# Kernel tuning notes

Hardware: AMD Instinct MI355X
Metric: run time of the kernel (lower is better)

Reference implementation:

```python
import jax, jax.numpy as jnp
import numpy as np

U, I, R, D = 100000, 50000, 5, 64
E_UI, E_UU = 1000000, 500000


def leaky(x, s):
    return jnp.where(x > 0, x, s * x)


def edge_softmax(scores, seg, n):
    # softmax over edges grouped by destination node (DGL edge_softmax)
    m = jax.ops.segment_max(scores, seg, num_segments=n)
    e = jnp.exp(scores - m[seg])
    s = jax.ops.segment_sum(e, seg, num_segments=n)
    return e / s[seg]


def attention(src, dst, w1, b1, w2, b2, w3, b3):
    # Attention module: relu(att1(cat)) -> relu(att2) -> att3 (dropout off: eval mode)
    x = jnp.concatenate([src, dst], axis=1)
    x = jax.nn.relu(x @ w1 + b1)
    x = jax.nn.relu(x @ w2 + b2)
    return (x @ w3 + b3)[:, 0]  # [E]


def setup_inputs() -> dict:
    key = jax.random.key(0)
    ks = iter(jax.random.split(key, 64))
    def p(*shape):
        return jax.random.normal(next(ks), shape, jnp.float32) * 0.05
    inp = {
        'user_emb': p(U, D), 'item_emb': p(I, D), 'rating_emb': p(R, D),
        'gv_w1': p(2 * D, D), 'gv_b1': p(D), 'gv_w2': p(D, D), 'gv_b2': p(D),
        'attI_w1': p(2 * D, D), 'attI_b1': p(D), 'attI_w2': p(D, D), 'attI_b2': p(D), 'attI_w3': p(D, 1), 'attI_b3': p(1),
        'wI_w': p(D, D), 'wI_b': p(D),
        'attS_w1': p(2 * D, D), 'attS_b1': p(D), 'attS_w2': p(D, D), 'attS_b2': p(D), 'attS_w3': p(D, 1), 'attS_b3': p(1),
        'wS_w': p(D, D), 'wS_b': p(D),
        'W2_w': p(2 * D, D), 'W2_b': p(D),
        'gu_w1': p(2 * D, D), 'gu_b1': p(D), 'gu_w2': p(D, D), 'gu_b2': p(D),
        'attU_w1': p(2 * D, D), 'attU_b1': p(D), 'attU_w2': p(D, D), 'attU_b2': p(D), 'attU_w3': p(D, 1), 'attU_b3': p(1),
        'wU_w': p(D, D), 'wU_b': p(D),
        'user_e': jax.random.randint(next(ks), (E_UI,), 0, U, jnp.int32),
        'item_e': jax.random.randint(next(ks), (E_UI,), 0, I, jnp.int32),
        'rating_e': jax.random.randint(next(ks), (E_UI,), 0, R, jnp.int32),
        'trust_e': jax.random.randint(next(ks), (E_UU,), 0, U, jnp.int32),
        'trustee_e': jax.random.randint(next(ks), (E_UU,), 0, U, jnp.int32),
    }
    return inp


def reference(user_emb, item_emb, rating_emb,
              gv_w1, gv_b1, gv_w2, gv_b2,
              attI_w1, attI_b1, attI_w2, attI_b2, attI_w3, attI_b3,
              wI_w, wI_b,
              attS_w1, attS_b1, attS_w2, attS_b2, attS_w3, attS_b3,
              wS_w, wS_b,
              W2_w, W2_b,
              gu_w1, gu_b1, gu_w2, gu_b2,
              attU_w1, attU_b1, attU_w2, attU_b2, attU_w3, attU_b3,
              wU_w, wU_b,
              user_e, item_e, rating_e, trust_e, trustee_e):
    act = lambda x: leaky(x, 0.2)  # LeakyReLU(0.2)

    # ---- ItemAgg: item->user edges, edge softmax over destination users ----
    i_e = item_emb[item_e]                     # [E_ui, D]
    u_e = user_emb[user_e]
    r_e = rating_emb[rating_e]
    x = jnp.concatenate([i_e, r_e], axis=1)    # gv MLP: LeakyReLU(0.01) default
    x = leaky(x @ gv_w1 + gv_b1, 0.01)
    x_ia = leaky(x @ gv_w2 + gv_b2, 0.01)
    sc = attention(x_ia, u_e, attI_w1, attI_b1, attI_w2, attI_b2, attI_w3, attI_b3)
    val = edge_softmax(sc, user_e, U)
    h = jax.ops.segment_sum(x_ia * val[:, None], user_e, num_segments=U)  # [U, D]
    hI = act(h @ wI_w + wI_b)

    # ---- SocialAgg: trust->trustee edges, softmax per trustee ----
    tr_e = user_emb[trust_e]
    te_e = hI[trustee_e]
    sc = attention(tr_e, te_e, attS_w1, attS_b1, attS_w2, attS_b2, attS_w3, attS_b3)
    val = edge_softmax(sc, trustee_e, U)
    # A.T @ hI: aggregate hi[trust] into trustee nodes with edge weights
    agg = jax.ops.segment_sum(val[:, None] * hI[trust_e], trustee_e, num_segments=U)
    hS = act(agg @ wS_w + wS_b)

    h_out = act(jnp.concatenate([hI, hS], axis=1) @ W2_w + W2_b)  # [U, D]

    # ---- UserAgg: user->item edges, softmax per destination item ----
    x = jnp.concatenate([user_emb[user_e], r_e], axis=1)
    x = jax.nn.relu(x @ gu_w1 + gu_b1)
    f_jt = jax.nn.relu(x @ gu_w2 + gu_b2)
    sc = attention(f_jt, i_e, attU_w1, attU_b1, attU_w2, attU_b2, attU_w3, attU_b3)
    val = edge_softmax(sc, item_e, I)
    z = jax.ops.segment_sum(f_jt * val[:, None], item_e, num_segments=I)  # [I, D]
    z = act(z @ wU_w + wU_b)

    return (h_out, z)
```

## Files before the change

### kernel.cpp

```cpp
#include <hip/hip_runtime.h>


typedef unsigned int   u32;
typedef unsigned short u16;
typedef short bf16x8 __attribute__((ext_vector_type(8)));
typedef float f32x4  __attribute__((ext_vector_type(4)));

#define U_N   100000
#define I_N   50000
#define EUI_E 1000000
#define EUU_E 500000
#define DOUT_ROWS 300000
#define RANGE 256
#define PB    256

__device__ __forceinline__ float bflo(u32 u){ return __uint_as_float(u << 16); }
__device__ __forceinline__ float bfhi(u32 u){ return __uint_as_float(u & 0xffff0000u); }
__device__ __forceinline__ u16 f2bf(float f){
  u32 x = __float_as_uint(f);
  x += 0x7fffu + ((x >> 16) & 1u);
  return (u16)(x >> 16);
}
__device__ __forceinline__ u32 pk2(float a, float b){
  return (u32)f2bf(a) | ((u32)f2bf(b) << 16);
}
__device__ __forceinline__ float actf(float x, float s){ return fmaxf(x, x * s); }
__device__ __forceinline__ void cvt8(uint4 q, float f[8]){
  f[0]=bflo(q.x); f[1]=bfhi(q.x); f[2]=bflo(q.y); f[3]=bfhi(q.y);
  f[4]=bflo(q.z); f[5]=bfhi(q.z); f[6]=bflo(q.w); f[7]=bfhi(q.w);
}

__device__ __forceinline__ bf16x8 bfrag(const float* __restrict__ W, int kt, int nt, int l){
  int c = l & 15, g = l >> 4;
  const float* p = W + (size_t)(kt*32 + g*8) * 64 + nt*16 + c;
  bf16x8 r;
  #pragma unroll
  for (int j = 0; j < 8; ++j) r[j] = (short)f2bf(p[(size_t)j * 64]);
  return r;
}
__device__ __forceinline__ bf16x8 afrag_f32(const float* p){
  float4 a = *(const float4*)p, b = *(const float4*)(p + 4);
  bf16x8 r;
  r[0]=(short)f2bf(a.x); r[1]=(short)f2bf(a.y); r[2]=(short)f2bf(a.z); r[3]=(short)f2bf(a.w);
  r[4]=(short)f2bf(b.x); r[5]=(short)f2bf(b.y); r[6]=(short)f2bf(b.z); r[7]=(short)f2bf(b.w);
  return r;
}
__device__ __forceinline__ bf16x8 afrag_f32s(const float* p, float s){
  float4 a = *(const float4*)p, b = *(const float4*)(p + 4);
  bf16x8 r;
  r[0]=(short)f2bf(a.x*s); r[1]=(short)f2bf(a.y*s); r[2]=(short)f2bf(a.z*s); r[3]=(short)f2bf(a.w*s);
  r[4]=(short)f2bf(b.x*s); r[5]=(short)f2bf(b.y*s); r[6]=(short)f2bf(b.z*s); r[7]=(short)f2bf(b.w*s);
  return r;
}
#define LDT 68
__device__ __forceinline__ void dwrite(float* lb, const f32x4* acc, float slope, int l){
  int c = l & 15, g = l >> 4;
  #pragma unroll
  for (int nt = 0; nt < 4; ++nt){
    #pragma unroll
    for (int rg = 0; rg < 4; ++rg)
      lb[(4*g + rg)*LDT + nt*16 + c] = actf(acc[nt][rg], slope);
  }
}
__device__ __forceinline__ bf16x8 afrag_lds(const float* lb, int kt, int l){
  int r = l & 15, g = l >> 4;
  return afrag_f32(lb + r*LDT + kt*32 + g*8);
}
__device__ __forceinline__ void store_rows2(const float* lb, u16* lo, u16* hi, int ndout,
                                            int base, int nrows, int l){
  int r = l >> 2, q = l & 3;
  if (r >= nrows) return;
  int row = base + r;
  u16* out = (row < ndout) ? lo + (size_t)row * 64 : hi + (size_t)(row - ndout) * 64;
  const float* src = lb + r*LDT + q*16;
  float4 a = *(const float4*)src, b = *(const float4*)(src+4);
  float4 c = *(const float4*)(src+8), d = *(const float4*)(src+12);
  uint4 w0, w1;
  w0.x = pk2(a.x,a.y); w0.y = pk2(a.z,a.w); w0.z = pk2(b.x,b.y); w0.w = pk2(b.z,b.w);
  w1.x = pk2(c.x,c.y); w1.y = pk2(c.z,c.w); w1.z = pk2(d.x,d.y); w1.w = pk2(d.z,d.w);
  u32* dst = (u32*)(out + (size_t)q*16);
  *(uint4*)dst = w0;
  *(uint4*)(dst + 4) = w1;
}
__device__ __forceinline__ void store_rows_f32(const float* lb, float* out,
                                               int base, int nrows, int l){
  int r = l >> 2, q = l & 3;
  if (r >= nrows) return;
  const float* src = lb + r*LDT + q*16;
  float* dst = out + (size_t)(base + r)*64 + q*16;
  *(float4*)(dst)    = *(const float4*)(src);
  *(float4*)(dst+4)  = *(const float4*)(src+4);
  *(float4*)(dst+8)  = *(const float4*)(src+8);
  *(float4*)(dst+12) = *(const float4*)(src+12);
}
#define MFMA(a,b,c) __builtin_amdgcn_mfma_f32_16x16x32_bf16((a),(b),(c),0,0,0)

__global__ void __launch_bounds__(256) mfma_pair_k(
    const float* __restrict__ embA, const float* __restrict__ embR,
    const float* __restrict__ W1, const float* __restrict__ b1,
    const float* __restrict__ W2, const float* __restrict__ b2,
    float slope, int plo, int phi, u16* __restrict__ Xlo, u16* __restrict__ Xhi, int ndout)
{
  __shared__ float lbuf[4][16*LDT];
  int l   = threadIdx.x & 63;
  int wid = threadIdx.x >> 6;
  float* lb = lbuf[wid];
  int c = l & 15;
  bf16x8 w1f[4][4], w2f[2][4];
  #pragma unroll
  for (int kt = 0; kt < 4; ++kt)
    #pragma unroll
    for (int nt = 0; nt < 4; ++nt) w1f[kt][nt] = bfrag(W1, kt, nt, l);
  #pragma unroll
  for (int kt = 0; kt < 2; ++kt)
    #pragma unroll
    for (int nt = 0; nt < 4; ++nt) w2f[kt][nt] = bfrag(W2, kt, nt, l);
  float bias1[4], bias2[4];
  #pragma unroll
  for (int nt = 0; nt < 4; ++nt){ bias1[nt] = b1[nt*16 + c]; bias2[nt] = b2[nt*16 + c]; }

  int n = phi - plo;
  int ngrp = (n + 15) >> 4;
  for (int grp = blockIdx.x*4 + wid; grp < ngrp; grp += gridDim.x*4){
    int base = grp * 16;
    int p = plo + base + (l & 15);
    if (p >= phi) p = phi - 1;
    int i = p / 5, r = p - 5*i;
    const float* ra = embA + (size_t)i * 64;
    const float* rr = embR + (size_t)r * 64;
    bf16x8 a0 = afrag_f32(ra + (l>>4)*8);
    bf16x8 a1 = afrag_f32(ra + 32 + (l>>4)*8);
    bf16x8 a2 = afrag_f32(rr + (l>>4)*8);
    bf16x8 a3 = afrag_f32(rr + 32 + (l>>4)*8);
    f32x4 acc[4];
    #pragma unroll
    for (int nt = 0; nt < 4; ++nt){
      f32x4 v; v[0]=bias1[nt]; v[1]=bias1[nt]; v[2]=bias1[nt]; v[3]=bias1[nt];
      v = MFMA(a0, w1f[0][nt], v);
      v = MFMA(a1, w1f[1][nt], v);
      v = MFMA(a2, w1f[2][nt], v);
      v = MFMA(a3, w1f[3][nt], v);
      acc[nt] = v;
    }
    dwrite(lb, acc, slope, l);
    bf16x8 x0 = afrag_lds(lb, 0, l);
    bf16x8 x1 = afrag_lds(lb, 1, l);
    #pragma unroll
    for (int nt = 0; nt < 4; ++nt){
      f32x4 v; v[0]=bias2[nt]; v[1]=bias2[nt]; v[2]=bias2[nt]; v[3]=bias2[nt];
      v = MFMA(x0, w2f[0][nt], v);
      v = MFMA(x1, w2f[1][nt], v);
      acc[nt] = v;
    }
    dwrite(lb, acc, slope, l);
    int nrows = n - base; if (nrows > 16) nrows = 16;
    store_rows2(lb, Xlo, Xhi, ndout, base, nrows, l);
  }
}

template<int AF32>
__global__ void __launch_bounds__(256) mfma_lin_k(
    const void* __restrict__ A, const float* __restrict__ W, const float* __restrict__ b,
    int has_bias, u16* __restrict__ out, int N)
{
  __shared__ float lbuf[4][16*LDT];
  int l   = threadIdx.x & 63;
  int wid = threadIdx.x >> 6;
  float* lb = lbuf[wid];
  int c = l & 15;
  bf16x8 wf[2][4];
  #pragma unroll
  for (int kt = 0; kt < 2; ++kt)
    #pragma unroll
    for (int nt = 0; nt < 4; ++nt) wf[kt][nt] = bfrag(W, kt, nt, l);
  float bias[4];
  #pragma unroll
  for (int nt = 0; nt < 4; ++nt) bias[nt] = has_bias ? b[nt*16 + c] : 0.0f;

  int ngrp = (N + 15) >> 4;
  for (int grp = blockIdx.x*4 + wid; grp < ngrp; grp += gridDim.x*4){
    int base = grp * 16;
    int ar = base + (l & 15);
    if (ar >= N) ar = N - 1;
    bf16x8 a0, a1;
    if (AF32){
      const float* row = (const float*)A + (size_t)ar * 64;
      a0 = afrag_f32(row + (l>>4)*8);
      a1 = afrag_f32(row + 32 + (l>>4)*8);
    } else {
      const u16* row = (const u16*)A + (size_t)ar * 64;
      a0 = *(const bf16x8*)(row + (l>>4)*8);
      a1 = *(const bf16x8*)(row + 32 + (l>>4)*8);
    }
    f32x4 acc[4];
    #pragma unroll
    for (int nt = 0; nt < 4; ++nt){
      f32x4 v; v[0]=bias[nt]; v[1]=bias[nt]; v[2]=bias[nt]; v[3]=bias[nt];
      v = MFMA(a0, wf[0][nt], v);
      v = MFMA(a1, wf[1][nt], v);
      acc[nt] = v;
    }
    dwrite(lb, acc, 1.0f, l);
    int nrows = N - base; if (nrows > 16) nrows = 16;
    store_rows2(lb, out, out, 1<<30, base, nrows, l);
  }
}

template<int OUTBF>
__global__ void __launch_bounds__(256) mfma_fin_k(
    const float* __restrict__ acc, const float* __restrict__ sdst,
    const float* __restrict__ W, const float* __restrict__ b,
    void* __restrict__ out, int N)
{
  __shared__ float lbuf[4][16*LDT];
  int l   = threadIdx.x & 63;
  int wid = threadIdx.x >> 6;
  float* lb = lbuf[wid];
  int r16 = l & 15, g = l >> 4;
  bf16x8 wf[2][4];
  #pragma unroll
  for (int kt = 0; kt < 2; ++kt)
    #pragma unroll
    for (int nt = 0; nt < 4; ++nt) wf[kt][nt] = bfrag(W, kt, nt, l);
  float bias[4];
  #pragma unroll
  for (int nt = 0; nt < 4; ++nt) bias[nt] = b[nt*16 + r16];

  int ngrp = (N + 15) >> 4;
  for (int grp = blockIdx.x*4 + wid; grp < ngrp; grp += gridDim.x*4){
    int base = grp * 16;
    int ar = base + r16; if (ar >= N) ar = N - 1;
    float s = sdst[ar];
    float inv = (s > 0.f) ? 1.0f / s : 0.0f;
    const float* row = acc + (size_t)ar * 64;
    bf16x8 a0 = afrag_f32s(row + g*8, inv);
    bf16x8 a1 = afrag_f32s(row + 32 + g*8, inv);
    f32x4 o[4];
    #pragma unroll
    for (int nt = 0; nt < 4; ++nt){
      f32x4 v; v[0]=bias[nt]; v[1]=bias[nt]; v[2]=bias[nt]; v[3]=bias[nt];
      v = MFMA(a0, wf[0][nt], v);
      v = MFMA(a1, wf[1][nt], v);
      o[nt] = v;
    }
    dwrite(lb, o, 0.2f, l);
    int nrows = N - base; if (nrows > 16) nrows = 16;
    if (OUTBF) store_rows2(lb, (u16*)out, (u16*)out, 1<<30, base, nrows, l);
    else       store_rows_f32(lb, (float*)out, base, nrows, l);
  }
}

__global__ void __launch_bounds__(256) mfma_fin_social_k(
    const float* __restrict__ accS, const float* __restrict__ sdst,
    const u16* __restrict__ hI,
    const float* __restrict__ wS, const float* __restrict__ bS,
    const float* __restrict__ W2, const float* __restrict__ b2,
    float* __restrict__ out, int N)
{
  __shared__ float lbuf[4][16*LDT];
  int l   = threadIdx.x & 63;
  int wid = threadIdx.x >> 6;
  float* lb = lbuf[wid];
  int r16 = l & 15, g = l >> 4;
  bf16x8 wsf[2][4], w2f[4][4];
  #pragma unroll
  for (int kt = 0; kt < 2; ++kt)
    #pragma unroll
    for (int nt = 0; nt < 4; ++nt) wsf[kt][nt] = bfrag(wS, kt, nt, l);
  #pragma unroll
  for (int kt = 0; kt < 4; ++kt)
    #pragma unroll
    for (int nt = 0; nt < 4; ++nt) w2f[kt][nt] = bfrag(W2, kt, nt, l);
  float biasS[4], bias2[4];
  #pragma unroll
  for (int nt = 0; nt < 4; ++nt){ biasS[nt] = bS[nt*16 + r16]; bias2[nt] = b2[nt*16 + r16]; }

  int ngrp = (N + 15) >> 4;
  for (int grp = blockIdx.x*4 + wid; grp < ngrp; grp += gridDim.x*4){
    int base = grp * 16;
    int ar = base + r16; if (ar >= N) ar = N - 1;
    float s = sdst[ar];
    float inv = (s > 0.f) ? 1.0f / s : 0.0f;
    const float* row = accS + (size_t)ar * 64;
    bf16x8 a0 = afrag_f32s(row + g*8, inv);
    bf16x8 a1 = afrag_f32s(row + 32 + g*8, inv);
    f32x4 hs[4];
    #pragma unroll
    for (int nt = 0; nt < 4; ++nt){
      f32x4 v; v[0]=biasS[nt]; v[1]=biasS[nt]; v[2]=biasS[nt]; v[3]=biasS[nt];
      v = MFMA(a0, wsf[0][nt], v);
      v = MFMA(a1, wsf[1][nt], v);
      hs[nt] = v;
    }
    dwrite(lb, hs, 0.2f, l);
    bf16x8 h0 = afrag_lds(lb, 0, l);
    bf16x8 h1 = afrag_lds(lb, 1, l);
    const u16* hrow = hI + (size_t)ar * 64;
    bf16x8 i0 = *(const bf16x8*)(hrow + g*8);
    bf16x8 i1 = *(const bf16x8*)(hrow + 32 + g*8);
    f32x4 o[4];
    #pragma unroll
    for (int nt = 0; nt < 4; ++nt){
      f32x4 v; v[0]=bias2[nt]; v[1]=bias2[nt]; v[2]=bias2[nt]; v[3]=bias2[nt];
      v = MFMA(i0, w2f[0][nt], v);
      v = MFMA(i1, w2f[1][nt], v);
      v = MFMA(h0, w2f[2][nt], v);
      v = MFMA(h1, w2f[3][nt], v);
      o[nt] = v;
    }
    dwrite(lb, o, 0.2f, l);
    int nrows = N - base; if (nrows > 16) nrows = 16;
    store_rows_f32(lb, out, base, nrows, l);
  }
}

__global__ void __launch_bounds__(256) hist2_k(const int* __restrict__ dstI, int E,
                                               int* __restrict__ H, int nb){
  __shared__ int h[512];
  for (int t = threadIdx.x; t < nb; t += 256) h[t] = 0;
  __syncthreads();
  int chunk = (E + PB - 1) / PB;
  int s = blockIdx.x * chunk;
  int e_end = s + chunk; if (e_end > E) e_end = E;
  for (int e = s + threadIdx.x; e < e_end; e += 256)
    atomicAdd(&h[dstI[e] >> 8], 1);
  __syncthreads();
  for (int t = threadIdx.x; t < nb; t += 256) H[t*PB + blockIdx.x] = h[t];
}
__global__ void __launch_bounds__(PB) totB_k(const int* __restrict__ H, int* __restrict__ tot){
  __shared__ int sh[PB];
  int b = blockIdx.x;
  sh[threadIdx.x] = H[b*PB + threadIdx.x];
  __syncthreads();
  for (int o = PB/2; o > 0; o >>= 1){
    if (threadIdx.x < o) sh[threadIdx.x] += sh[threadIdx.x + o];
    __syncthreads();
  }
  if (threadIdx.x == 0) tot[b] = sh[0];
}
__global__ void __launch_bounds__(512) scanB_k(const int* __restrict__ tot,
                                               int* __restrict__ baseB, int nb){
  __shared__ int sh[512];
  int v = (threadIdx.x < nb) ? tot[threadIdx.x] : 0;
  sh[threadIdx.x] = v;
  __syncthreads();
  for (int o = 1; o < 512; o <<= 1){
    int t = (threadIdx.x >= o) ? sh[threadIdx.x - o] : 0;
    __syncthreads();
    sh[threadIdx.x] += t;
    __syncthreads();
  }
  if (threadIdx.x < nb) baseB[threadIdx.x] = sh[threadIdx.x] - v;
  if (threadIdx.x == nb - 1) baseB[nb] = sh[threadIdx.x];
}
__global__ void __launch_bounds__(PB) offB_k(int* __restrict__ H, const int* __restrict__ baseB){
  __shared__ int sh[PB];
  int b = blockIdx.x;
  int v = H[b*PB + threadIdx.x];
  sh[threadIdx.x] = v;
  __syncthreads();
  for (int o = 1; o < PB; o <<= 1){
    int t = (threadIdx.x >= o) ? sh[threadIdx.x - o] : 0;
    __syncthreads();
    sh[threadIdx.x] += t;
    __syncthreads();
  }
  H[b*PB + threadIdx.x] = baseB[b] + sh[threadIdx.x] - v;
}
__global__ void __launch_bounds__(256) part_k(
    const int* __restrict__ keyI, const int* __restrict__ ratI, int kmul,
    const int* __restrict__ dstI, const int* __restrict__ H, int nb,
    long long* __restrict__ kd2, int E){
  __shared__ int cur[512];
  for (int t = threadIdx.x; t < nb; t += 256) cur[t] = H[t*PB + blockIdx.x];
  __syncthreads();
  int chunk = (E + PB - 1) / PB;
  int s = blockIdx.x * chunk;
  int e_end = s + chunk; if (e_end > E) e_end = E;
  for (int e = s + threadIdx.x; e < e_end; e += 256){
    int d = dstI[e];
    int key = keyI[e]*kmul + (ratI ? ratI[e] : 0);
    int pos = atomicAdd(&cur[d >> 8], 1);
    long long v = ((long long)d << 32) | (unsigned)key;
    __builtin_nontemporal_store(v, kd2 + pos);
  }
}
__global__ void __launch_bounds__(256) bsort_k(
    const long long* __restrict__ kd2, const int* __restrict__ baseB,
    int N, long long* __restrict__ kd, int* __restrict__ rowptr, int E){
  __shared__ int cnt[RANGE];
  __shared__ int off[RANGE];
  int b = blockIdx.x;
  int lo = baseB[b], hi = baseB[b+1];
  cnt[threadIdx.x] = 0;
  __syncthreads();
  for (int k = lo + (int)threadIdx.x; k < hi; k += 256){
    int d = (int)(kd2[k] >> 32);
    atomicAdd(&cnt[d & 255], 1);
  }
  __syncthreads();
  int v = cnt[threadIdx.x];
  off[threadIdx.x] = v;
  __syncthreads();
  for (int o = 1; o < RANGE; o <<= 1){
    int t = (threadIdx.x >= o) ? off[threadIdx.x - o] : 0;
    __syncthreads();
    off[threadIdx.x] += t;
    __syncthreads();
  }
  int excl = off[threadIdx.x] - v;
  int d0 = b*RANGE + (int)threadIdx.x;
  if (d0 < N) rowptr[d0] = lo + excl;
  if (b == (int)gridDim.x - 1 && threadIdx.x == 0) rowptr[N] = E;
  __syncthreads();
  cnt[threadIdx.x] = lo + excl;
  __syncthreads();
  for (int k = lo + (int)threadIdx.x; k < hi; k += 256){
    long long v2 = kd2[k];
    int d = (int)(v2 >> 32);
    int pos = atomicAdd(&cnt[d & 255], 1);
    kd[pos] = v2;
  }
}

template<int CY>
__global__ void __launch_bounds__(256) fscore_k(
    const int2* __restrict__ kd,
    const u16* __restrict__ Xlo, const u16* __restrict__ Xhi, int ndout,
    int klo, int nk,
    const u16* __restrict__ Dtab,
    const float* __restrict__ Wy,
    const float* __restrict__ W2, const float* __restrict__ b2,
    const float* __restrict__ w3, const float* __restrict__ b3,
    float* __restrict__ esc, int E)
{
  __shared__ float lbuf[4][16*LDT];
  int l   = threadIdx.x & 63;
  int wid = threadIdx.x >> 6;
  int r16 = l & 15, g = l >> 4;
  float* lb = lbuf[wid];
  bf16x8 wyf[2][4], w2f[2][4];
  if (CY){
    #pragma unroll
    for (int kt = 0; kt < 2; ++kt)
      #pragma unroll
      for (int nt = 0; nt < 4; ++nt) wyf[kt][nt] = bfrag(Wy, kt, nt, l);
  }
  #pragma unroll
  for (int kt = 0; kt < 2; ++kt)
    #pragma unroll
    for (int nt = 0; nt < 4; ++nt) w2f[kt][nt] = bfrag(W2, kt, nt, l);
  f32x4 b2v[4]; float w3v[4];
  #pragma unroll
  for (int nt = 0; nt < 4; ++nt){
    float bv = b2[nt*16 + r16];
    f32x4 t; t[0]=bv; t[1]=bv; t[2]=bv; t[3]=bv;
    b2v[nt] = t;
    w3v[nt] = w3[nt*16 + r16];
  }
  float b3v = b3[0];

  int ngrp = (E + 15) >> 4;
  for (int grp = blockIdx.x*4 + wid; grp < ngrp; grp += gridDim.x*4){
    int pos = grp*16 + r16;
    int pc  = pos < E ? pos : E - 1;
    int2 kde = kd[pc];
    int j   = kde.x - klo;
    bool inr = (pos < E) && ((unsigned)j < (unsigned)nk);
    unsigned long long bal = __ballot(inr ? 1 : 0);
    uint4 xa = {0,0,0,0}, xb = xa, da = xa, db = xa;
    if (inr){
      const u16* xr = (j < ndout) ? Xlo + (size_t)j * 64 : Xhi + (size_t)(j - ndout) * 64;
      xa = *(const uint4*)(xr + g*8);
      xb = *(const uint4*)(xr + 32 + g*8);
      const u16* dr = Dtab + (size_t)kde.y * 64;
      da = *(const uint4*)(dr + g*8);
      db = *(const uint4*)(dr + 32 + g*8);
    }
    bf16x8 p0, p1;
    float dfa[8], dfb[8];
    cvt8(da, dfa); cvt8(db, dfb);
    if (CY){
      bf16x8 a0 = *reinterpret_cast<const bf16x8*>(&xa);
      bf16x8 a1 = *reinterpret_cast<const bf16x8*>(&xb);
      f32x4 y[4];
      #pragma unroll
      for (int nt = 0; nt < 4; ++nt){
        f32x4 z; z[0]=0.f; z[1]=0.f; z[2]=0.f; z[3]=0.f;
        z = MFMA(a0, wyf[0][nt], z);
        z = MFMA(a1, wyf[1][nt], z);
        y[nt] = z;
      }
      #pragma unroll
      for (int nt = 0; nt < 4; ++nt)
        #pragma unroll
        for (int rg = 0; rg < 4; ++rg)
          lb[(4*g + rg)*LDT + nt*16 + r16] = y[nt][rg];
      const float* pr = lb + r16*LDT;
      float4 f0 = *(const float4*)(pr + g*8);
      float4 f1 = *(const float4*)(pr + g*8 + 4);
      float4 f2 = *(const float4*)(pr + 32 + g*8);
      float4 f3 = *(const float4*)(pr + 36 + g*8);
      float q0[8] = {f0.x,f0.y,f0.z,f0.w,f1.x,f1.y,f1.z,f1.w};
      float q1[8] = {f2.x,f2.y,f2.z,f2.w,f3.x,f3.y,f3.z,f3.w};
      #pragma unroll
      for (int u = 0; u < 8; ++u){
        p0[u] = (short)f2bf(fmaxf(q0[u] + dfa[u], 0.0f));
        p1[u] = (short)f2bf(fmaxf(q1[u] + dfb[u], 0.0f));
      }
    } else {
      float xfa[8], xfb[8];
      cvt8(xa, xfa); cvt8(xb, xfb);
      #pragma unroll
      for (int u = 0; u < 8; ++u){
        p0[u] = (short)f2bf(fmaxf(xfa[u] + dfa[u], 0.0f));
        p1[u] = (short)f2bf(fmaxf(xfb[u] + dfb[u], 0.0f));
      }
    }
    f32x4 o[4];
    #pragma unroll
    for (int nt = 0; nt < 4; ++nt){
      f32x4 v = b2v[nt];
      v = MFMA(p0, w2f[0][nt], v);
      v = MFMA(p1, w2f[1][nt], v);
      o[nt] = v;
    }
    float part[4] = {0.f, 0.f, 0.f, 0.f};
    #pragma unroll
    for (int nt = 0; nt < 4; ++nt)
      #pragma unroll
      for (int rg = 0; rg < 4; ++rg)
        part[rg] += fmaxf(o[nt][rg], 0.0f) * w3v[nt];
    #pragma unroll
    for (int m = 1; m < 16; m <<= 1){
      #pragma unroll
      for (int rg = 0; rg < 4; ++rg) part[rg] += __shfl_xor(part[rg], m);
    }
    if (r16 < 4){
      int eidx = 4*g + r16;
      int p2 = grp*16 + eidx;
      if (p2 < E && ((bal >> eidx) & 1))
        esc[p2] = __expf(part[r16] + b3v);
    }
  }
}

template<int FIRST>
__global__ void __launch_bounds__(256) agg4_k(
    const int* __restrict__ rowptr, const int2* __restrict__ kd,
    const float* __restrict__ esc,
    const u16* __restrict__ Xlo, const u16* __restrict__ Xhi, int ndout,
    int klo, int nk,
    float* __restrict__ acc, float* __restrict__ sdst, int N)
{
  int t = blockIdx.x*256 + threadIdx.x;
  int d = t >> 2, q = t & 3;
  if (d >= N) return;
  float a[16];
  float* ar = acc + (size_t)d * 64 + q*16;
  float s;
  if (FIRST){
    #pragma unroll
    for (int u = 0; u < 16; ++u) a[u] = 0.0f;
    s = 0.0f;
  } else {
    #pragma unroll
    for (int u = 0; u < 16; u += 4){
      float4 v = *(const float4*)(ar + u);
      a[u]=v.x; a[u+1]=v.y; a[u+2]=v.z; a[u+3]=v.w;
    }
    s = sdst[d];
  }
  int k0 = rowptr[d], k1 = rowptr[d+1];
  for (int k = k0; k < k1; ++k){
    int key = kd[k].x - klo;
    if ((unsigned)key >= (unsigned)nk) continue;
    float w = esc[k];
    s += w;
    const u16* xr = ((key < ndout) ? Xlo + (size_t)key * 64
                                   : Xhi + (size_t)(key - ndout) * 64) + q*16;
    uint4 q0 = *(const uint4*)xr;
    uint4 q1 = *(const uint4*)(xr + 8);
    float f0[8], f1[8]; cvt8(q0, f0); cvt8(q1, f1);
    #pragma unroll
    for (int u = 0; u < 8; ++u){
      a[u]     = fmaf(w, f0[u], a[u]);
      a[u + 8] = fmaf(w, f1[u], a[u + 8]);
    }
  }
  #pragma unroll
  for (int u = 0; u < 16; u += 4)
    *(float4*)(ar + u) = make_float4(a[u], a[u+1], a[u+2], a[u+3]);
  if (q == 0) sdst[d] = s;
}

extern "C" void kernel_launch(void* const* d_in, const int* in_sizes, int n_in,
                              void* d_out, int out_size, void* d_ws, size_t ws_size,
                              hipStream_t stream) {
  (void)in_sizes; (void)n_in; (void)out_size;
  const float* user_emb   = (const float*)d_in[0];
  const float* item_emb   = (const float*)d_in[1];
  const float* rating_emb = (const float*)d_in[2];
  const float *gv_w1=(const float*)d_in[3],  *gv_b1=(const float*)d_in[4];
  const float *gv_w2=(const float*)d_in[5],  *gv_b2=(const float*)d_in[6];
  const float *aI_w1=(const float*)d_in[7],  *aI_b1=(const float*)d_in[8];
  const float *aI_w2=(const float*)d_in[9],  *aI_b2=(const float*)d_in[10];
  const float *aI_w3=(const float*)d_in[11], *aI_b3=(const float*)d_in[12];
  const float *wI_w =(const float*)d_in[13], *wI_b =(const float*)d_in[14];
  const float *aS_w1=(const float*)d_in[15], *aS_b1=(const float*)d_in[16];
  const float *aS_w2=(const float*)d_in[17], *aS_b2=(const float*)d_in[18];
  const float *aS_w3=(const float*)d_in[19], *aS_b3=(const float*)d_in[20];
  const float *wS_w =(const float*)d_in[21], *wS_b =(const float*)d_in[22];
  const float *W2_w =(const float*)d_in[23], *W2_b =(const float*)d_in[24];
  const float *gu_w1=(const float*)d_in[25], *gu_b1=(const float*)d_in[26];
  const float *gu_w2=(const float*)d_in[27], *gu_b2=(const float*)d_in[28];
  const float *aU_w1=(const float*)d_in[29], *aU_b1=(const float*)d_in[30];
  const float *aU_w2=(const float*)d_in[31], *aU_b2=(const float*)d_in[32];
  const float *aU_w3=(const float*)d_in[33], *aU_b3=(const float*)d_in[34];
  const float *wU_w =(const float*)d_in[35], *wU_b =(const float*)d_in[36];
  const int* user_e    = (const int*)d_in[37];
  const int* item_e    = (const int*)d_in[38];
  const int* rating_e  = (const int*)d_in[39];
  const int* trust_e   = (const int*)d_in[40];
  const int* trustee_e = (const int*)d_in[41];
  float* dout = (float*)d_out;

  char* base = (char*)d_ws;
  size_t cur = 0;
  auto alloc = [&](size_t bytes)->char*{
    char* p = base + cur; cur += (bytes + 255) & ~(size_t)255; return p;
  };
  u16*   hI     = (u16*)  alloc((size_t)U_N * 64 * 2);
  float* esc    = (float*)alloc((size_t)EUI_E * 4);
  float* sdst   = (float*)alloc((size_t)U_N * 4);
  int*   rowptr = (int*)  alloc((size_t)(U_N + 1) * 4);
  int2*  kd     = (int2*) alloc((size_t)EUI_E * 8);
  int*   H      = (int*)  alloc((size_t)512 * PB * 4);
  int*   tot    = (int*)  alloc(512 * 4);
  int*   baseB  = (int*)  alloc(513 * 4);
  float* acc    = (float*)alloc((size_t)U_N * 64 * 4);
  long long* kd2 = (long long*)acc;
  size_t fixed_end = cur;
  if (ws_size < fixed_end + 13100000) return;
  u16* tabD = (u16*)(base + fixed_end);
  u16* tabX = (u16*)(base + fixed_end + 6500352);
  size_t arena = ws_size - fixed_end;
  u16* Xdout = (u16*)d_out;

  auto cdiv = [](int a, int b){ return (a + b - 1) / b; };
  auto buildCSR = [&](const int* keyI, const int* ratI, int kmul,
                      const int* dstIdx, int E, int N){
    int nb = cdiv(N, RANGE);
    hist2_k<<<PB, 256, 0, stream>>>(dstIdx, E, H, nb);
    totB_k<<<nb, PB, 0, stream>>>(H, tot);
    scanB_k<<<1, 512, 0, stream>>>(tot, baseB, nb);
    offB_k<<<nb, PB, 0, stream>>>(H, baseB);
    part_k<<<PB, 256, 0, stream>>>(keyI, ratI, kmul, dstIdx, H, nb, kd2, E);
    bsort_k<<<nb, 256, 0, stream>>>(kd2, baseB, N, (long long*)kd, rowptr, E);
  };
  auto gCap = [&](int groups){ int g = cdiv(groups, 4); return g > 1536 ? 1536 : g; };

  {
    buildCSR(item_e, rating_e, 5, user_e, EUI_E, U_N);
    mfma_lin_k<1><<<gCap(cdiv(U_N,16)), 256, 0, stream>>>(user_emb, aI_w1 + 64*64, aI_b1, 1, tabD, U_N);
    const int NK = 250000;
    mfma_pair_k<<<gCap(cdiv(NK,16)), 256, 0, stream>>>(item_emb, rating_emb,
        gv_w1, gv_b1, gv_w2, gv_b2, 0.01f, 0, NK, Xdout, Xdout, 1<<30);
    fscore_k<1><<<gCap(cdiv(EUI_E,16)), 256, 0, stream>>>(kd,
        Xdout, Xdout, 1<<30, 0, NK, tabD, aI_w1, aI_w2, aI_b2, aI_w3, aI_b3, esc, EUI_E);
    agg4_k<1><<<cdiv(U_N*4,256), 256, 0, stream>>>(rowptr, kd, esc,
        Xdout, Xdout, 1<<30, 0, NK, acc, sdst, U_N);
    mfma_fin_k<1><<<gCap(cdiv(U_N,16)), 256, 0, stream>>>(acc, sdst, wI_w, wI_b, hI, U_N);
  }

  {
    buildCSR(user_e, rating_e, 5, item_e, EUI_E, I_N);
    mfma_lin_k<1><<<gCap(cdiv(I_N,16)), 256, 0, stream>>>(item_emb, aU_w1 + 64*64, aU_b1, 1, tabD, I_N);
    bool single = arena >= 33000000;
    int CP = single ? 500000 : 250000;
    int ND = single ? DOUT_ROWS : (1<<30);
    for (int klo = 0; klo < 500000; klo += CP){
      mfma_pair_k<<<gCap(cdiv(CP,16)), 256, 0, stream>>>(user_emb, rating_emb,
          gu_w1, gu_b1, gu_w2, gu_b2, 0.0f, klo, klo + CP, Xdout, tabX, ND);
      fscore_k<1><<<gCap(cdiv(EUI_E,16)), 256, 0, stream>>>(kd,
          Xdout, tabX, ND, klo, CP, tabD, aU_w1, aU_w2, aU_b2, aU_w3, aU_b3, esc, EUI_E);
      if (klo == 0)
        agg4_k<1><<<cdiv(I_N*4,256), 256, 0, stream>>>(rowptr, kd, esc,
            Xdout, tabX, ND, klo, CP, acc, sdst, I_N);
      else
        agg4_k<0><<<cdiv(I_N*4,256), 256, 0, stream>>>(rowptr, kd, esc,
            Xdout, tabX, ND, klo, CP, acc, sdst, I_N);
    }
    mfma_fin_k<0><<<gCap(cdiv(I_N,16)), 256, 0, stream>>>(acc, sdst, wU_w, wU_b,
        dout + (size_t)U_N * 64, I_N);
  }

  {
    buildCSR(trust_e, (const int*)nullptr, 1, trustee_e, EUU_E, U_N);
    u16* SD = Xdout;
    mfma_lin_k<1><<<gCap(cdiv(U_N,16)), 256, 0, stream>>>(user_emb, aS_w1, aS_b1, 0, tabD, U_N);
    mfma_lin_k<0><<<gCap(cdiv(U_N,16)), 256, 0, stream>>>(hI, aS_w1 + 64*64, aS_b1, 1, SD, U_N);
    fscore_k<0><<<gCap(cdiv(EUU_E,16)), 256, 0, stream>>>(kd,
        tabD, tabD, 1<<30, 0, U_N, SD, (const float*)nullptr,
        aS_w2, aS_b2, aS_w3, aS_b3, esc, EUU_E);
    agg4_k<1><<<cdiv(U_N*4,256), 256, 0, stream>>>(rowptr, kd, esc,
        hI, hI, 1<<30, 0, U_N, acc, sdst, U_N);
    mfma_fin_social_k<<<gCap(cdiv(U_N,16)), 256, 0, stream>>>(acc, sdst, hI,
        wS_w, wS_b, W2_w, W2_b, dout, U_N);
  }
}
```

Before: 507.1 us.

## Prefetch next edge group in fscore and use 8 threads per node in aggregation

The edge-scoring kernel now software-pipelines its grid-stride loop, issuing the gathers for the next 16-edge group before computing the current one so that gather latency overlaps the MFMA work. The aggregation kernel moves from 4 to 8 threads per destination node, each handling 8 features, and prefetches the next edge's row and weight while accumulating the current one. The non-MFMA fscore variant also stops allocating the unused LDS buffer. The cost is higher register pressure from the double-buffered loads and twice as many threads in aggregation, each reloading the rowptr and edge keys.

```diff
diff --git a/kernel.cpp b/kernel.cpp
--- a/kernel.cpp
+++ b/kernel.cpp
@@ -434,11 +434,11 @@
     const float* __restrict__ w3, const float* __restrict__ b3,
     float* __restrict__ esc, int E)
 {
-  __shared__ float lbuf[4][16*LDT];
+  __shared__ float lbuf[CY ? 4*16*LDT : 4];
   int l   = threadIdx.x & 63;
   int wid = threadIdx.x >> 6;
   int r16 = l & 15, g = l >> 4;
-  float* lb = lbuf[wid];
+  float* lb = lbuf + (CY ? wid*16*LDT : 0);
   bf16x8 wyf[2][4], w2f[2][4];
   if (CY){
     #pragma unroll
@@ -461,22 +461,38 @@
   float b3v = b3[0];
 
   int ngrp = (E + 15) >> 4;
-  for (int grp = blockIdx.x*4 + wid; grp < ngrp; grp += gridDim.x*4){
-    int pos = grp*16 + r16;
+  int stride = gridDim.x*4;
+  int grp = blockIdx.x*4 + wid;
+  if (grp >= ngrp) return;
+
+  auto loadg = [&](int gg, int2& kde_, bool& inr_,
+                   uint4& xa_, uint4& xb_, uint4& da_, uint4& db_){
+    int pos = gg*16 + r16;
     int pc  = pos < E ? pos : E - 1;
-    int2 kde = kd[pc];
-    int j   = kde.x - klo;
-    bool inr = (pos < E) && ((unsigned)j < (unsigned)nk);
+    kde_ = kd[pc];
+    int j = kde_.x - klo;
+    inr_ = (pos < E) && ((unsigned)j < (unsigned)nk);
+    uint4 z = {0,0,0,0};
+    xa_ = z; xb_ = z; da_ = z; db_ = z;
+    if (inr_){
+      const u16* xr = (j < ndout) ? Xlo + (size_t)j * 64 : Xhi + (size_t)(j - ndout) * 64;
+      xa_ = *(const uint4*)(xr + g*8);
+      xb_ = *(const uint4*)(xr + 32 + g*8);
+      const u16* dr = Dtab + (size_t)kde_.y * 64;
+      da_ = *(const uint4*)(dr + g*8);
+      db_ = *(const uint4*)(dr + 32 + g*8);
+    }
+  };
+
+  int2 kde; bool inr; uint4 xa, xb, da, db;
+  loadg(grp, kde, inr, xa, xb, da, db);
+
+  while (true){
+    int gn = grp + stride;
+    int2 kde_n; bool inr_n = false; uint4 xa_n, xb_n, da_n, db_n;
+    if (gn < ngrp) loadg(gn, kde_n, inr_n, xa_n, xb_n, da_n, db_n);
+
     unsigned long long bal = __ballot(inr ? 1 : 0);
-    uint4 xa = {0,0,0,0}, xb = xa, da = xa, db = xa;
-    if (inr){
-      const u16* xr = (j < ndout) ? Xlo + (size_t)j * 64 : Xhi + (size_t)(j - ndout) * 64;
-      xa = *(const uint4*)(xr + g*8);
-      xb = *(const uint4*)(xr + 32 + g*8);
-      const u16* dr = Dtab + (size_t)kde.y * 64;
-      da = *(const uint4*)(dr + g*8);
-      db = *(const uint4*)(dr + 32 + g*8);
-    }
     bf16x8 p0, p1;
     float dfa[8], dfb[8];
     cvt8(da, dfa); cvt8(db, dfb);
@@ -542,11 +558,14 @@
       if (p2 < E && ((bal >> eidx) & 1))
         esc[p2] = __expf(part[r16] + b3v);
     }
+    if (gn >= ngrp) break;
+    grp = gn; kde = kde_n; inr = inr_n;
+    xa = xa_n; xb = xb_n; da = da_n; db = db_n;
   }
 }
 
 template<int FIRST>
-__global__ void __launch_bounds__(256) agg4_k(
+__global__ void __launch_bounds__(256) agg8_k(
     const int* __restrict__ rowptr, const int2* __restrict__ kd,
     const float* __restrict__ esc,
     const u16* __restrict__ Xlo, const u16* __restrict__ Xhi, int ndout,
@@ -554,43 +573,52 @@
     float* __restrict__ acc, float* __restrict__ sdst, int N)
 {
   int t = blockIdx.x*256 + threadIdx.x;
-  int d = t >> 2, q = t & 3;
+  int d = t >> 3, q = t & 7;
   if (d >= N) return;
-  float a[16];
-  float* ar = acc + (size_t)d * 64 + q*16;
+  float a[8];
+  float* ar = acc + (size_t)d * 64 + q*8;
   float s;
   if (FIRST){
     #pragma unroll
-    for (int u = 0; u < 16; ++u) a[u] = 0.0f;
+    for (int u = 0; u < 8; ++u) a[u] = 0.0f;
     s = 0.0f;
   } else {
-    #pragma unroll
-    for (int u = 0; u < 16; u += 4){
-      float4 v = *(const float4*)(ar + u);
-      a[u]=v.x; a[u+1]=v.y; a[u+2]=v.z; a[u+3]=v.w;
-    }
+    float4 v0 = *(const float4*)(ar);
+    float4 v1 = *(const float4*)(ar + 4);
+    a[0]=v0.x; a[1]=v0.y; a[2]=v0.z; a[3]=v0.w;
+    a[4]=v1.x; a[5]=v1.y; a[6]=v1.z; a[7]=v1.w;
     s = sdst[d];
   }
   int k0 = rowptr[d], k1 = rowptr[d+1];
-  for (int k = k0; k < k1; ++k){
-    int key = kd[k].x - klo;
-    if ((unsigned)key >= (unsigned)nk) continue;
-    float w = esc[k];
+  auto xrow = [&](int key)->const u16*{
+    return ((key < ndout) ? Xlo + (size_t)key * 64
+                          : Xhi + (size_t)(key - ndout) * 64) + q*8;
+  };
+  if (k0 < k1){
+    int key = kd[k0].x - klo;
+    bool ok = (unsigned)key < (unsigned)nk;
+    float w = ok ? esc[k0] : 0.0f;
+    uint4 x = {0,0,0,0};
+    if (ok) x = *(const uint4*)xrow(key);
+    for (int k = k0 + 1; k < k1; ++k){
+      int key2 = kd[k].x - klo;
+      bool ok2 = (unsigned)key2 < (unsigned)nk;
+      float w2 = ok2 ? esc[k] : 0.0f;
+      uint4 x2 = {0,0,0,0};
+      if (ok2) x2 = *(const uint4*)xrow(key2);
+      s += w;
+      float f[8]; cvt8(x, f);
+      #pragma unroll
+      for (int u = 0; u < 8; ++u) a[u] = fmaf(w, f[u], a[u]);
+      x = x2; w = w2;
+    }
     s += w;
-    const u16* xr = ((key < ndout) ? Xlo + (size_t)key * 64
-                                   : Xhi + (size_t)(key - ndout) * 64) + q*16;
-    uint4 q0 = *(const uint4*)xr;
-    uint4 q1 = *(const uint4*)(xr + 8);
-    float f0[8], f1[8]; cvt8(q0, f0); cvt8(q1, f1);
-    #pragma unroll
-    for (int u = 0; u < 8; ++u){
-      a[u]     = fmaf(w, f0[u], a[u]);
-      a[u + 8] = fmaf(w, f1[u], a[u + 8]);
-    }
-  }
-  #pragma unroll
-  for (int u = 0; u < 16; u += 4)
-    *(float4*)(ar + u) = make_float4(a[u], a[u+1], a[u+2], a[u+3]);
+    float f[8]; cvt8(x, f);
+    #pragma unroll
+    for (int u = 0; u < 8; ++u) a[u] = fmaf(w, f[u], a[u]);
+  }
+  *(float4*)(ar)     = make_float4(a[0], a[1], a[2], a[3]);
+  *(float4*)(ar + 4) = make_float4(a[4], a[5], a[6], a[7]);
   if (q == 0) sdst[d] = s;
 }
 
@@ -668,7 +696,7 @@
         gv_w1, gv_b1, gv_w2, gv_b2, 0.01f, 0, NK, Xdout, Xdout, 1<<30);
     fscore_k<1><<<gCap(cdiv(EUI_E,16)), 256, 0, stream>>>(kd,
         Xdout, Xdout, 1<<30, 0, NK, tabD, aI_w1, aI_w2, aI_b2, aI_w3, aI_b3, esc, EUI_E);
-    agg4_k<1><<<cdiv(U_N*4,256), 256, 0, stream>>>(rowptr, kd, esc,
+    agg8_k<1><<<cdiv(U_N*8,256), 256, 0, stream>>>(rowptr, kd, esc,
         Xdout, Xdout, 1<<30, 0, NK, acc, sdst, U_N);
     mfma_fin_k<1><<<gCap(cdiv(U_N,16)), 256, 0, stream>>>(acc, sdst, wI_w, wI_b, hI, U_N);
   }
@@ -685,10 +713,10 @@
       fscore_k<1><<<gCap(cdiv(EUI_E,16)), 256, 0, stream>>>(kd,
           Xdout, tabX, ND, klo, CP, tabD, aU_w1, aU_w2, aU_b2, aU_w3, aU_b3, esc, EUI_E);
       if (klo == 0)
-        agg4_k<1><<<cdiv(I_N*4,256), 256, 0, stream>>>(rowptr, kd, esc,
+        agg8_k<1><<<cdiv(I_N*8,256), 256, 0, stream>>>(rowptr, kd, esc,
             Xdout, tabX, ND, klo, CP, acc, sdst, I_N);
       else
-        agg4_k<0><<<cdiv(I_N*4,256), 256, 0, stream>>>(rowptr, kd, esc,
+        agg8_k<0><<<cdiv(I_N*8,256), 256, 0, stream>>>(rowptr, kd, esc,
             Xdout, tabX, ND, klo, CP, acc, sdst, I_N);
     }
     mfma_fin_k<0><<<gCap(cdiv(I_N,16)), 256, 0, stream>>>(acc, sdst, wU_w, wU_b,
@@ -703,7 +731,7 @@
     fscore_k<0><<<gCap(cdiv(EUU_E,16)), 256, 0, stream>>>(kd,
         tabD, tabD, 1<<30, 0, U_N, SD, (const float*)nullptr,
         aS_w2, aS_b2, aS_w3, aS_b3, esc, EUU_E);
-    agg4_k<1><<<cdiv(U_N*4,256), 256, 0, stream>>>(rowptr, kd, esc,
+    agg8_k<1><<<cdiv(U_N*8,256), 256, 0, stream>>>(rowptr, kd, esc,
         hI, hI, 1<<30, 0, U_N, acc, sdst, U_N);
     mfma_fin_social_k<<<gCap(cdiv(U_N,16)), 256, 0, stream>>>(acc, sdst, hI,
         wS_w, wS_b, W2_w, W2_b, dout, U_N);
```

Result: slower. 524.2 us (+3.4%).
